# Kernel tuning notes

Measured on AMD Instinct MI355X. Metric: run time of the kernel, lower is better.

The kernel has to match this reference:

```python
import jax, jax.numpy as jnp
import numpy as np

NUM_HEADS = 16
DIM_K = 64
EMB_DIM = 1024
NEG_INF = -1.0e9


def setup_inputs() -> dict:
    key = jax.random.key(0)
    ks = jax.random.split(key, 12)
    B, Sq, Skv, D = 2, 2048, 2048, EMB_DIM
    HDK = NUM_HEADS * DIM_K
    s = 1.0 / np.sqrt(D)
    return {
        "q": jax.random.normal(ks[0], (B, Sq, D), jnp.float32),
        "k": jax.random.normal(ks[1], (B, Skv, D), jnp.float32),
        "v": jax.random.normal(ks[2], (B, Skv, D), jnp.float32),
        "mask": jax.random.randint(ks[3], (B, 1, Skv), 0, 2, jnp.int32),
        "Wq": jax.random.normal(ks[4], (D, HDK), jnp.float32) * s,
        "bq": jnp.zeros((HDK,), jnp.float32),
        "Wk": jax.random.normal(ks[5], (D, HDK), jnp.float32) * s,
        "bk": jnp.zeros((HDK,), jnp.float32),
        "Wv": jax.random.normal(ks[6], (D, HDK), jnp.float32) * s,
        "bv": jnp.zeros((HDK,), jnp.float32),
        "Wo": jax.random.normal(ks[7], (HDK, D), jnp.float32) * (1.0 / np.sqrt(HDK)),
        "bo": jnp.zeros((D,), jnp.float32),
    }


def reference(q, k, v, mask, Wq, bq, Wk, bk, Wv, bv, Wo, bo):
    B, Sq, _ = q.shape
    Skv = k.shape[1]
    H, dk = NUM_HEADS, DIM_K
    # projections  (B,S,D) -> (B,H,S,dk)
    qh = (q @ Wq + bq).reshape(B, Sq, H, dk).transpose(0, 2, 1, 3)
    kh = (k @ Wk + bk).reshape(B, Skv, H, dk).transpose(0, 2, 1, 3)
    vh = (v @ Wv + bv).reshape(B, Skv, H, dk).transpose(0, 2, 1, 3)
    # scores (B,H,Sq,Skv)
    scores = jnp.einsum("bhqd,bhkd->bhqk", qh, kh) / jnp.float32(np.sqrt(dk))
    # mask (B,1,Skv) -> (B,1,1,Skv); masked_fill where mask == 0
    scores = jnp.where(mask[:, None] == 0, jnp.float32(NEG_INF), scores)
    probs = jax.nn.softmax(scores, axis=-1)  # dropout is identity in eval
    attn = jnp.einsum("bhqk,bhkd->bhqd", probs, vh)
    concat = attn.transpose(0, 2, 1, 3).reshape(B, Sq, H * dk)
    output = concat @ Wo + bo
    return output, scores
```

## Files before the change

### kernel.cpp

```cpp
#include <hip/hip_runtime.h>
#include <hip/hip_bf16.h>

typedef __attribute__((ext_vector_type(8))) short short8;
typedef __attribute__((ext_vector_type(4))) float f32x4;
typedef __hip_bfloat16 bf16;

#define NH 16
#define DK 64
#define SEQ 2048
#define DIM 1024
#define NEG_INF_F (-1.0e9f)

static __device__ __forceinline__ unsigned short f2bf_bits(float f) {
    bf16 t = __float2bfloat16(f);
    return *reinterpret_cast<unsigned short*>(&t);
}

__global__ void cvt_all_kernel(const float* __restrict__ q, const float* __restrict__ k,
                               const float* __restrict__ v, bf16* __restrict__ qb,
                               bf16* __restrict__ kb, bf16* __restrict__ vb) {
    const int N4 = 2 * SEQ * DIM / 4;
    int i = blockIdx.x * blockDim.x + threadIdx.x;
    int sel = i / N4, j = i - sel * N4;
    const float* in = (sel == 0) ? q : (sel == 1) ? k : v;
    bf16* out = (sel == 0) ? qb : (sel == 1) ? kb : vb;
    float4 x = reinterpret_cast<const float4*>(in)[j];
    ushort4 u;
    u.x = f2bf_bits(x.x);
    u.y = f2bf_bits(x.y);
    u.z = f2bf_bits(x.z);
    u.w = f2bf_bits(x.w);
    reinterpret_cast<ushort4*>(out)[j] = u;
}

__global__ void transpose_cvt_kernel(const float* __restrict__ Wq, const float* __restrict__ Wk,
                                     const float* __restrict__ Wv, const float* __restrict__ Wo,
                                     bf16* __restrict__ Wqt, bf16* __restrict__ Wkt,
                                     bf16* __restrict__ Wvt, bf16* __restrict__ Wot) {
    __shared__ float t[32][33];
    const int z = blockIdx.z;
    const float* W = (z == 0) ? Wq : (z == 1) ? Wk : (z == 2) ? Wv : Wo;
    bf16* Wt = (z == 0) ? Wqt : (z == 1) ? Wkt : (z == 2) ? Wvt : Wot;
    int n0 = blockIdx.x * 32, k0 = blockIdx.y * 32;
    int tx = threadIdx.x, ty = threadIdx.y;
#pragma unroll
    for (int i = 0; i < 4; i++)
        t[ty + i * 8][tx] = W[(size_t)(k0 + ty + i * 8) * DIM + n0 + tx];
    __syncthreads();
#pragma unroll
    for (int i = 0; i < 4; i++)
        Wt[(size_t)(n0 + ty + i * 8) * DIM + k0 + tx] = __float2bfloat16(t[tx][ty + i * 8]);
}

__global__ __launch_bounds__(256) void qkv_gemm_kernel(
    const bf16* __restrict__ qb, const bf16* __restrict__ kb, const bf16* __restrict__ vb,
    const bf16* __restrict__ Wcat,
    const float* __restrict__ bq, const float* __restrict__ bk, const float* __restrict__ bv,
    bf16* __restrict__ Qh, bf16* __restrict__ Kh, bf16* __restrict__ Vt)
{
    __shared__ __align__(16) bf16 Xs[2][128 * 40];
    __shared__ __align__(16) bf16 Ws[2][128 * 40];
    const int tid = threadIdx.x;
    const int w = tid >> 6, l = tid & 63;
    const int l15 = l & 15, l4 = l >> 4;
    const int lin = blockIdx.x;
    const int swz = (lin & 7) * 96 + (lin >> 3);
    const int proj = swz >> 8;
    const int rem = swz & 255;
    const int m0 = (rem >> 3) * 128;
    const int n0 = (rem & 7) * 128;
    const bf16* X = (proj == 0) ? qb : (proj == 1) ? kb : vb;
    const bf16* Wt = Wcat + (size_t)proj * DIM * DIM + (size_t)n0 * DIM;
    const float* bias = (proj == 0) ? bq : (proj == 1) ? bk : bv;
    const int wr = w >> 1, wc = w & 1;
    f32x4 acc[4][4] = {};

    const int c0 = tid, c1 = 256 + tid;
    const int r0 = c0 >> 2, ch0 = c0 & 3;
    const int r1 = c1 >> 2, ch1 = c1 & 3;
    const bf16* Xp = X + (size_t)m0 * DIM;

    short8 x0 = *reinterpret_cast<const short8*>(&Xp[(size_t)r0 * DIM + ch0 * 8]);
    short8 x1 = *reinterpret_cast<const short8*>(&Xp[(size_t)r1 * DIM + ch1 * 8]);
    short8 w0 = *reinterpret_cast<const short8*>(&Wt[(size_t)r0 * DIM + ch0 * 8]);
    short8 w1 = *reinterpret_cast<const short8*>(&Wt[(size_t)r1 * DIM + ch1 * 8]);
    *reinterpret_cast<short8*>(&Xs[0][r0 * 40 + ch0 * 8]) = x0;
    *reinterpret_cast<short8*>(&Xs[0][r1 * 40 + ch1 * 8]) = x1;
    *reinterpret_cast<short8*>(&Ws[0][r0 * 40 + ch0 * 8]) = w0;
    *reinterpret_cast<short8*>(&Ws[0][r1 * 40 + ch1 * 8]) = w1;
    __syncthreads();

    int cur = 0;
    for (int k0 = 0; k0 < DIM; k0 += 32) {
        const bool more = (k0 + 32) < DIM;
        short8 nx0, nx1, nw0, nw1;
        if (more) {
            nx0 = *reinterpret_cast<const short8*>(&Xp[(size_t)r0 * DIM + k0 + 32 + ch0 * 8]);
            nx1 = *reinterpret_cast<const short8*>(&Xp[(size_t)r1 * DIM + k0 + 32 + ch1 * 8]);
            nw0 = *reinterpret_cast<const short8*>(&Wt[(size_t)r0 * DIM + k0 + 32 + ch0 * 8]);
            nw1 = *reinterpret_cast<const short8*>(&Wt[(size_t)r1 * DIM + k0 + 32 + ch1 * 8]);
        }
        short8 af[4], bfr[4];
#pragma unroll
        for (int mi = 0; mi < 4; mi++)
            af[mi] = *reinterpret_cast<const short8*>(&Xs[cur][(wr * 64 + mi * 16 + l15) * 40 + l4 * 8]);
#pragma unroll
        for (int ni = 0; ni < 4; ni++)
            bfr[ni] = *reinterpret_cast<const short8*>(&Ws[cur][(wc * 64 + ni * 16 + l15) * 40 + l4 * 8]);
#pragma unroll
        for (int mi = 0; mi < 4; mi++)
#pragma unroll
            for (int ni = 0; ni < 4; ni++)
                acc[mi][ni] = __builtin_amdgcn_mfma_f32_16x16x32_bf16(af[mi], bfr[ni], acc[mi][ni], 0, 0, 0);
        if (more) {
            *reinterpret_cast<short8*>(&Xs[cur ^ 1][r0 * 40 + ch0 * 8]) = nx0;
            *reinterpret_cast<short8*>(&Xs[cur ^ 1][r1 * 40 + ch1 * 8]) = nx1;
            *reinterpret_cast<short8*>(&Ws[cur ^ 1][r0 * 40 + ch0 * 8]) = nw0;
            *reinterpret_cast<short8*>(&Ws[cur ^ 1][r1 * 40 + ch1 * 8]) = nw1;
        }
        __syncthreads();
        cur ^= 1;
    }

#pragma unroll
    for (int mi = 0; mi < 4; mi++) {
#pragma unroll
        for (int ni = 0; ni < 4; ni++) {
            int n = n0 + wc * 64 + ni * 16 + l15;
            float bv = bias[n];
            int h = n >> 6, d = n & 63;
#pragma unroll
            for (int j = 0; j < 4; j++) {
                int m = m0 + wr * 64 + mi * 16 + l4 * 4 + j;
                float val = acc[mi][ni][j] + bv;
                int b = m >> 11, s = m & 2047;
                if (proj == 0)
                    Qh[((size_t)(b * NH + h) * SEQ + s) * DK + d] = __float2bfloat16(val * 0.125f);
                else if (proj == 1)
                    Kh[((size_t)(b * NH + h) * SEQ + s) * DK + d] = __float2bfloat16(val);
                else
                    Vt[((size_t)(b * NH + h) * DK + d) * SEQ + s] = __float2bfloat16(val);
            }
        }
    }
}

__global__ __launch_bounds__(256) void o_gemm_kernel(
    const bf16* __restrict__ X, const bf16* __restrict__ Wt,
    const float* __restrict__ bias, float* __restrict__ out)
{
    __shared__ __align__(16) bf16 Xs[2][64 * 40];
    __shared__ __align__(16) bf16 Ws[2][128 * 40];
    const int tid = threadIdx.x;
    const int w = tid >> 6, l = tid & 63;
    const int l15 = l & 15, l4 = l >> 4;
    const int lin = blockIdx.x;
    const int swz = (lin & 7) * 64 + (lin >> 3);
    const int m0 = (swz >> 3) * 64;
    const int n0 = (swz & 7) * 128;
    const int wr = w >> 1, wc = w & 1;
    f32x4 acc[2][4] = {};

    const int xr = tid >> 2, xc = tid & 3;
    const int c0 = tid, c1 = 256 + tid;
    const int wr0 = c0 >> 2, wc0 = c0 & 3;
    const int wr1 = c1 >> 2, wc1 = c1 & 3;
    const bf16* Xp = X + (size_t)m0 * DIM;
    const bf16* Wp = Wt + (size_t)n0 * DIM;

    short8 x0 = *reinterpret_cast<const short8*>(&Xp[(size_t)xr * DIM + xc * 8]);
    short8 w0 = *reinterpret_cast<const short8*>(&Wp[(size_t)wr0 * DIM + wc0 * 8]);
    short8 w1 = *reinterpret_cast<const short8*>(&Wp[(size_t)wr1 * DIM + wc1 * 8]);
    *reinterpret_cast<short8*>(&Xs[0][xr * 40 + xc * 8]) = x0;
    *reinterpret_cast<short8*>(&Ws[0][wr0 * 40 + wc0 * 8]) = w0;
    *reinterpret_cast<short8*>(&Ws[0][wr1 * 40 + wc1 * 8]) = w1;
    __syncthreads();

    int cur = 0;
    for (int k0 = 0; k0 < DIM; k0 += 32) {
        const bool more = (k0 + 32) < DIM;
        short8 nx0, nw0, nw1;
        if (more) {
            nx0 = *reinterpret_cast<const short8*>(&Xp[(size_t)xr * DIM + k0 + 32 + xc * 8]);
            nw0 = *reinterpret_cast<const short8*>(&Wp[(size_t)wr0 * DIM + k0 + 32 + wc0 * 8]);
            nw1 = *reinterpret_cast<const short8*>(&Wp[(size_t)wr1 * DIM + k0 + 32 + wc1 * 8]);
        }
        short8 af[2], bfr[4];
#pragma unroll
        for (int mi = 0; mi < 2; mi++)
            af[mi] = *reinterpret_cast<const short8*>(&Xs[cur][(wr * 32 + mi * 16 + l15) * 40 + l4 * 8]);
#pragma unroll
        for (int ni = 0; ni < 4; ni++)
            bfr[ni] = *reinterpret_cast<const short8*>(&Ws[cur][(wc * 64 + ni * 16 + l15) * 40 + l4 * 8]);
#pragma unroll
        for (int mi = 0; mi < 2; mi++)
#pragma unroll
            for (int ni = 0; ni < 4; ni++)
                acc[mi][ni] = __builtin_amdgcn_mfma_f32_16x16x32_bf16(af[mi], bfr[ni], acc[mi][ni], 0, 0, 0);
        if (more) {
            *reinterpret_cast<short8*>(&Xs[cur ^ 1][xr * 40 + xc * 8]) = nx0;
            *reinterpret_cast<short8*>(&Ws[cur ^ 1][wr0 * 40 + wc0 * 8]) = nw0;
            *reinterpret_cast<short8*>(&Ws[cur ^ 1][wr1 * 40 + wc1 * 8]) = nw1;
        }
        __syncthreads();
        cur ^= 1;
    }

#pragma unroll
    for (int mi = 0; mi < 2; mi++) {
#pragma unroll
        for (int ni = 0; ni < 4; ni++) {
            int n = n0 + wc * 64 + ni * 16 + l15;
            float bv = bias[n];
#pragma unroll
            for (int j = 0; j < 4; j++) {
                int m = m0 + wr * 32 + mi * 16 + l4 * 4 + j;
                out[(size_t)m * DIM + n] = acc[mi][ni][j] + bv;
            }
        }
    }
}

__global__ __launch_bounds__(256) void attn_kernel(
    const bf16* __restrict__ Qh, const bf16* __restrict__ Kh,
    const bf16* __restrict__ Vt, const int* __restrict__ mask,
    float* __restrict__ scores, bf16* __restrict__ attn_c)
{
    __shared__ __align__(16) bf16 Ks[2][64 * 72];
    __shared__ __align__(16) bf16 Vs[2][64 * 72];
    __shared__ __align__(16) bf16 Ps[128 * 72];
    __shared__ int msk_s[SEQ];
    const int tid = threadIdx.x;
    const int w = tid >> 6, l = tid & 63;
    const int l15 = l & 15, l4 = l >> 4;
    const int lin = blockIdx.x;
    const int swz = (lin & 7) * 64 + (lin >> 3);
    const int bh = swz >> 4;
    const int q0 = (swz & 15) * 128;
    const int b = bh >> 4, h = bh & 15;
    const size_t head = (size_t)bh * SEQ * DK;

    const int c0 = tid, c1 = 256 + tid;
    const int kr0 = c0 >> 3, kc0 = c0 & 7;
    const int kr1 = c1 >> 3, kc1 = c1 & 7;

    short8 aq[2][2];
#pragma unroll
    for (int mi = 0; mi < 2; mi++)
#pragma unroll
        for (int ks = 0; ks < 2; ks++)
            aq[mi][ks] = *reinterpret_cast<const short8*>(
                &Qh[head + (size_t)(q0 + w * 32 + mi * 16 + l15) * DK + ks * 32 + l4 * 8]);

    {
        const int4* msrc = reinterpret_cast<const int4*>(mask + b * SEQ);
#pragma unroll
        for (int i = 0; i < 2; i++)
            reinterpret_cast<int4*>(msk_s)[i * 256 + tid] = msrc[i * 256 + tid];
        short8 k0v = *reinterpret_cast<const short8*>(&Kh[head + (size_t)kr0 * DK + kc0 * 8]);
        short8 k1v = *reinterpret_cast<const short8*>(&Kh[head + (size_t)kr1 * DK + kc1 * 8]);
        short8 v0v = *reinterpret_cast<const short8*>(&Vt[head + (size_t)kr0 * SEQ + kc0 * 8]);
        short8 v1v = *reinterpret_cast<const short8*>(&Vt[head + (size_t)kr1 * SEQ + kc1 * 8]);
        *reinterpret_cast<short8*>(&Ks[0][kr0 * 72 + kc0 * 8]) = k0v;
        *reinterpret_cast<short8*>(&Ks[0][kr1 * 72 + kc1 * 8]) = k1v;
        *reinterpret_cast<short8*>(&Vs[0][kr0 * 72 + kc0 * 8]) = v0v;
        *reinterpret_cast<short8*>(&Vs[0][kr1 * 72 + kc1 * 8]) = v1v;
    }
    __syncthreads();

    f32x4 oacc[2][4] = {};
    float mrun[2][4], lrun[2][4];
#pragma unroll
    for (int mi = 0; mi < 2; mi++)
#pragma unroll
        for (int j = 0; j < 4; j++) { mrun[mi][j] = -INFINITY; lrun[mi][j] = 0.f; }

    int cur = 0;
    for (int t = 0; t < SEQ / 64; t++) {
        const int kv0 = t * 64;
        const bool more = t < (SEQ / 64 - 1);
        short8 nk0, nk1, nv0, nv1;
        if (more) {
            nk0 = *reinterpret_cast<const short8*>(&Kh[head + (size_t)(kv0 + 64 + kr0) * DK + kc0 * 8]);
            nk1 = *reinterpret_cast<const short8*>(&Kh[head + (size_t)(kv0 + 64 + kr1) * DK + kc1 * 8]);
            nv0 = *reinterpret_cast<const short8*>(&Vt[head + (size_t)kr0 * SEQ + kv0 + 64 + kc0 * 8]);
            nv1 = *reinterpret_cast<const short8*>(&Vt[head + (size_t)kr1 * SEQ + kv0 + 64 + kc1 * 8]);
        }

        f32x4 sacc[2][4] = {};
#pragma unroll
        for (int ks = 0; ks < 2; ks++) {
            short8 bk[4];
#pragma unroll
            for (int ni = 0; ni < 4; ni++)
                bk[ni] = *reinterpret_cast<const short8*>(&Ks[cur][(ni * 16 + l15) * 72 + ks * 32 + l4 * 8]);
#pragma unroll
            for (int mi = 0; mi < 2; mi++)
#pragma unroll
                for (int ni = 0; ni < 4; ni++)
                    sacc[mi][ni] = __builtin_amdgcn_mfma_f32_16x16x32_bf16(aq[mi][ks], bk[ni], sacc[mi][ni], 0, 0, 0);
        }

        int mk[4];
#pragma unroll
        for (int ni = 0; ni < 4; ni++) mk[ni] = msk_s[kv0 + ni * 16 + l15];
#pragma unroll
        for (int mi = 0; mi < 2; mi++)
#pragma unroll
            for (int ni = 0; ni < 4; ni++)
                if (mk[ni] == 0) {
#pragma unroll
                    for (int j = 0; j < 4; j++) sacc[mi][ni][j] = NEG_INF_F;
                }

        {
            size_t base = ((size_t)bh * SEQ + q0 + w * 32) * SEQ + kv0;
#pragma unroll
            for (int mi = 0; mi < 2; mi++)
#pragma unroll
                for (int j = 0; j < 4; j++) {
                    size_t rb = base + (size_t)(mi * 16 + l4 * 4 + j) * SEQ;
#pragma unroll
                    for (int ni = 0; ni < 4; ni++)
                        __builtin_nontemporal_store(sacc[mi][ni][j], &scores[rb + ni * 16 + l15]);
                }
        }

#pragma unroll
        for (int mi = 0; mi < 2; mi++)
#pragma unroll
            for (int j = 0; j < 4; j++) {
                float mx = fmaxf(fmaxf(sacc[mi][0][j], sacc[mi][1][j]),
                                 fmaxf(sacc[mi][2][j], sacc[mi][3][j]));
#pragma unroll
                for (int d = 1; d < 16; d <<= 1) mx = fmaxf(mx, __shfl_xor(mx, d));
                if (mx > mrun[mi][j]) {
                    float fac = __expf(mrun[mi][j] - mx);
                    lrun[mi][j] *= fac;
#pragma unroll
                    for (int ni = 0; ni < 4; ni++) oacc[mi][ni][j] *= fac;
                    mrun[mi][j] = mx;
                }
                float mcur = mrun[mi][j];
                float ps = 0.f;
#pragma unroll
                for (int ni = 0; ni < 4; ni++) {
                    float p = __expf(sacc[mi][ni][j] - mcur);
                    sacc[mi][ni][j] = p;
                    ps += p;
                }
                lrun[mi][j] += ps;
            }

#pragma unroll
        for (int mi = 0; mi < 2; mi++)
#pragma unroll
            for (int j = 0; j < 4; j++) {
                int r = w * 32 + mi * 16 + l4 * 4 + j;
#pragma unroll
                for (int ni = 0; ni < 4; ni++)
                    Ps[r * 72 + ni * 16 + l15] = __float2bfloat16(sacc[mi][ni][j]);
            }

#pragma unroll
        for (int ks = 0; ks < 2; ks++) {
            short8 pa[2], vbf[4];
#pragma unroll
            for (int mi = 0; mi < 2; mi++)
                pa[mi] = *reinterpret_cast<const short8*>(&Ps[(w * 32 + mi * 16 + l15) * 72 + ks * 32 + l4 * 8]);
#pragma unroll
            for (int ni = 0; ni < 4; ni++)
                vbf[ni] = *reinterpret_cast<const short8*>(&Vs[cur][(ni * 16 + l15) * 72 + ks * 32 + l4 * 8]);
#pragma unroll
            for (int mi = 0; mi < 2; mi++)
#pragma unroll
                for (int ni = 0; ni < 4; ni++)
                    oacc[mi][ni] = __builtin_amdgcn_mfma_f32_16x16x32_bf16(pa[mi], vbf[ni], oacc[mi][ni], 0, 0, 0);
        }

        if (more) {
            *reinterpret_cast<short8*>(&Ks[cur ^ 1][kr0 * 72 + kc0 * 8]) = nk0;
            *reinterpret_cast<short8*>(&Ks[cur ^ 1][kr1 * 72 + kc1 * 8]) = nk1;
            *reinterpret_cast<short8*>(&Vs[cur ^ 1][kr0 * 72 + kc0 * 8]) = nv0;
            *reinterpret_cast<short8*>(&Vs[cur ^ 1][kr1 * 72 + kc1 * 8]) = nv1;
        }
        __syncthreads();
        cur ^= 1;
    }

#pragma unroll
    for (int mi = 0; mi < 2; mi++)
#pragma unroll
        for (int j = 0; j < 4; j++) {
            float ls = lrun[mi][j];
#pragma unroll
            for (int d = 1; d < 16; d <<= 1) ls += __shfl_xor(ls, d);
            float inv = 1.f / ls;
            int s = q0 + w * 32 + mi * 16 + l4 * 4 + j;
#pragma unroll
            for (int ni = 0; ni < 4; ni++)
                attn_c[((size_t)(b * SEQ + s)) * DIM + h * DK + ni * 16 + l15] =
                    __float2bfloat16(oacc[mi][ni][j] * inv);
        }
}

extern "C" void kernel_launch(void* const* d_in, const int* in_sizes, int n_in,
                              void* d_out, int out_size, void* d_ws, size_t ws_size,
                              hipStream_t stream)
{
    const float* q  = (const float*)d_in[0];
    const float* k  = (const float*)d_in[1];
    const float* v  = (const float*)d_in[2];
    const int*  msk = (const int*)d_in[3];
    const float* Wq = (const float*)d_in[4];
    const float* bq = (const float*)d_in[5];
    const float* Wk = (const float*)d_in[6];
    const float* bk = (const float*)d_in[7];
    const float* Wv = (const float*)d_in[8];
    const float* bv = (const float*)d_in[9];
    const float* Wo = (const float*)d_in[10];
    const float* bo = (const float*)d_in[11];

    const size_t MB = 1ull << 20;
    char* ws = (char*)d_ws;
    bf16* qb  = (bf16*)(ws + 0 * MB);
    bf16* kb  = (bf16*)(ws + 8 * MB);
    bf16* vb  = (bf16*)(ws + 16 * MB);
    bf16* Wqt = (bf16*)(ws + 24 * MB);
    bf16* Wkt = (bf16*)(ws + 26 * MB);
    bf16* Wvt = (bf16*)(ws + 28 * MB);
    bf16* Wot = (bf16*)(ws + 30 * MB);
    bf16* QhD = (bf16*)(ws + 32 * MB);
    bf16* KhD = (bf16*)(ws + 40 * MB);
    bf16* VtD = (bf16*)(ws + 48 * MB);
    bf16* att = (bf16*)(ws + 56 * MB);

    float* out = (float*)d_out;
    float* scores = out + (size_t)4096 * 1024;

    cvt_all_kernel<<<3 * 4096, 256, 0, stream>>>(q, k, v, qb, kb, vb);
    transpose_cvt_kernel<<<dim3(32, 32, 4), dim3(32, 8), 0, stream>>>(
        Wq, Wk, Wv, Wo, Wqt, Wkt, Wvt, Wot);

    qkv_gemm_kernel<<<768, 256, 0, stream>>>(qb, kb, vb, Wqt, bq, bk, bv, QhD, KhD, VtD);

    attn_kernel<<<512, 256, 0, stream>>>(QhD, KhD, VtD, msk, scores, att);

    o_gemm_kernel<<<512, 256, 0, stream>>>(att, Wot, bo, out);
}
```

Before: 240.2 us.

## Load K/V fragments directly from global into registers, dropping LDS staging

The attention kernel no longer stages K and V tiles in double-buffered shared memory. Each wave now reads its MFMA operand fragments straight from global memory: K is prefetched one tile ahead into registers, V is loaded at the top of each iteration, and the mask is read from global instead of shared. This removes the LDS writes, the per-iteration block barrier and most of the shared-memory footprint, which could allow more resident blocks. In exchange, every wave fetches the whole K/V tile itself, roughly four times the L2 traffic, and uses more registers.

```diff
diff --git a/kernel.cpp b/kernel.cpp
--- a/kernel.cpp
+++ b/kernel.cpp
@@ -226,10 +226,7 @@
     const bf16* __restrict__ Vt, const int* __restrict__ mask,
     float* __restrict__ scores, bf16* __restrict__ attn_c)
 {
-    __shared__ __align__(16) bf16 Ks[2][64 * 72];
-    __shared__ __align__(16) bf16 Vs[2][64 * 72];
     __shared__ __align__(16) bf16 Ps[128 * 72];
-    __shared__ int msk_s[SEQ];
     const int tid = threadIdx.x;
     const int w = tid >> 6, l = tid & 63;
     const int l15 = l & 15, l4 = l >> 4;
@@ -240,10 +237,6 @@
     const int b = bh >> 4, h = bh & 15;
     const size_t head = (size_t)bh * SEQ * DK;
 
-    const int c0 = tid, c1 = 256 + tid;
-    const int kr0 = c0 >> 3, kc0 = c0 & 7;
-    const int kr1 = c1 >> 3, kc1 = c1 & 7;
-
     short8 aq[2][2];
 #pragma unroll
     for (int mi = 0; mi < 2; mi++)
@@ -252,21 +245,17 @@
             aq[mi][ks] = *reinterpret_cast<const short8*>(
                 &Qh[head + (size_t)(q0 + w * 32 + mi * 16 + l15) * DK + ks * 32 + l4 * 8]);
 
-    {
-        const int4* msrc = reinterpret_cast<const int4*>(mask + b * SEQ);
-#pragma unroll
-        for (int i = 0; i < 2; i++)
-            reinterpret_cast<int4*>(msk_s)[i * 256 + tid] = msrc[i * 256 + tid];
-        short8 k0v = *reinterpret_cast<const short8*>(&Kh[head + (size_t)kr0 * DK + kc0 * 8]);
-        short8 k1v = *reinterpret_cast<const short8*>(&Kh[head + (size_t)kr1 * DK + kc1 * 8]);
-        short8 v0v = *reinterpret_cast<const short8*>(&Vt[head + (size_t)kr0 * SEQ + kc0 * 8]);
-        short8 v1v = *reinterpret_cast<const short8*>(&Vt[head + (size_t)kr1 * SEQ + kc1 * 8]);
-        *reinterpret_cast<short8*>(&Ks[0][kr0 * 72 + kc0 * 8]) = k0v;
-        *reinterpret_cast<short8*>(&Ks[0][kr1 * 72 + kc1 * 8]) = k1v;
-        *reinterpret_cast<short8*>(&Vs[0][kr0 * 72 + kc0 * 8]) = v0v;
-        *reinterpret_cast<short8*>(&Vs[0][kr1 * 72 + kc1 * 8]) = v1v;
-    }
-    __syncthreads();
+    const bf16* Kp = Kh + head;
+    const bf16* Vp = Vt + head;
+    const int* mrow = mask + b * SEQ;
+
+    short8 kf[2][4];
+#pragma unroll
+    for (int ks = 0; ks < 2; ks++)
+#pragma unroll
+        for (int ni = 0; ni < 4; ni++)
+            kf[ks][ni] = *reinterpret_cast<const short8*>(
+                &Kp[(size_t)(ni * 16 + l15) * DK + ks * 32 + l4 * 8]);
 
     f32x4 oacc[2][4] = {};
     float mrun[2][4], lrun[2][4];
@@ -275,35 +264,38 @@
 #pragma unroll
         for (int j = 0; j < 4; j++) { mrun[mi][j] = -INFINITY; lrun[mi][j] = 0.f; }
 
-    int cur = 0;
     for (int t = 0; t < SEQ / 64; t++) {
         const int kv0 = t * 64;
-        const bool more = t < (SEQ / 64 - 1);
-        short8 nk0, nk1, nv0, nv1;
-        if (more) {
-            nk0 = *reinterpret_cast<const short8*>(&Kh[head + (size_t)(kv0 + 64 + kr0) * DK + kc0 * 8]);
-            nk1 = *reinterpret_cast<const short8*>(&Kh[head + (size_t)(kv0 + 64 + kr1) * DK + kc1 * 8]);
-            nv0 = *reinterpret_cast<const short8*>(&Vt[head + (size_t)kr0 * SEQ + kv0 + 64 + kc0 * 8]);
-            nv1 = *reinterpret_cast<const short8*>(&Vt[head + (size_t)kr1 * SEQ + kv0 + 64 + kc1 * 8]);
-        }
+
+        short8 vf[2][4];
+#pragma unroll
+        for (int ks = 0; ks < 2; ks++)
+#pragma unroll
+            for (int ni = 0; ni < 4; ni++)
+                vf[ks][ni] = *reinterpret_cast<const short8*>(
+                    &Vp[(size_t)(ni * 16 + l15) * SEQ + kv0 + ks * 32 + l4 * 8]);
 
         f32x4 sacc[2][4] = {};
 #pragma unroll
-        for (int ks = 0; ks < 2; ks++) {
-            short8 bk[4];
-#pragma unroll
-            for (int ni = 0; ni < 4; ni++)
-                bk[ni] = *reinterpret_cast<const short8*>(&Ks[cur][(ni * 16 + l15) * 72 + ks * 32 + l4 * 8]);
+        for (int ks = 0; ks < 2; ks++)
 #pragma unroll
             for (int mi = 0; mi < 2; mi++)
 #pragma unroll
                 for (int ni = 0; ni < 4; ni++)
-                    sacc[mi][ni] = __builtin_amdgcn_mfma_f32_16x16x32_bf16(aq[mi][ks], bk[ni], sacc[mi][ni], 0, 0, 0);
+                    sacc[mi][ni] = __builtin_amdgcn_mfma_f32_16x16x32_bf16(aq[mi][ks], kf[ks][ni], sacc[mi][ni], 0, 0, 0);
+
+        if (t < SEQ / 64 - 1) {
+#pragma unroll
+            for (int ks = 0; ks < 2; ks++)
+#pragma unroll
+                for (int ni = 0; ni < 4; ni++)
+                    kf[ks][ni] = *reinterpret_cast<const short8*>(
+                        &Kp[(size_t)(kv0 + 64 + ni * 16 + l15) * DK + ks * 32 + l4 * 8]);
         }
 
         int mk[4];
 #pragma unroll
-        for (int ni = 0; ni < 4; ni++) mk[ni] = msk_s[kv0 + ni * 16 + l15];
+        for (int ni = 0; ni < 4; ni++) mk[ni] = mrow[kv0 + ni * 16 + l15];
 #pragma unroll
         for (int mi = 0; mi < 2; mi++)
 #pragma unroll
@@ -364,28 +356,16 @@
 
 #pragma unroll
         for (int ks = 0; ks < 2; ks++) {
-            short8 pa[2], vbf[4];
+            short8 pa[2];
 #pragma unroll
             for (int mi = 0; mi < 2; mi++)
                 pa[mi] = *reinterpret_cast<const short8*>(&Ps[(w * 32 + mi * 16 + l15) * 72 + ks * 32 + l4 * 8]);
 #pragma unroll
-            for (int ni = 0; ni < 4; ni++)
-                vbf[ni] = *reinterpret_cast<const short8*>(&Vs[cur][(ni * 16 + l15) * 72 + ks * 32 + l4 * 8]);
-#pragma unroll
             for (int mi = 0; mi < 2; mi++)
 #pragma unroll
                 for (int ni = 0; ni < 4; ni++)
-                    oacc[mi][ni] = __builtin_amdgcn_mfma_f32_16x16x32_bf16(pa[mi], vbf[ni], oacc[mi][ni], 0, 0, 0);
-        }
-
-        if (more) {
-            *reinterpret_cast<short8*>(&Ks[cur ^ 1][kr0 * 72 + kc0 * 8]) = nk0;
-            *reinterpret_cast<short8*>(&Ks[cur ^ 1][kr1 * 72 + kc1 * 8]) = nk1;
-            *reinterpret_cast<short8*>(&Vs[cur ^ 1][kr0 * 72 + kc0 * 8]) = nv0;
-            *reinterpret_cast<short8*>(&Vs[cur ^ 1][kr1 * 72 + kc1 * 8]) = nv1;
-        }
-        __syncthreads();
-        cur ^= 1;
+                    oacc[mi][ni] = __builtin_amdgcn_mfma_f32_16x16x32_bf16(pa[mi], vf[ks][ni], oacc[mi][ni], 0, 0, 0);
+        }
     }
 
 #pragma unroll
```

Result: slower. 283.3 us (+17.9%).
